# Kernel optimization log

Hardware: AMD Instinct MI355X
Metric: run time of the kernel (lower is better)

Reference implementation:

```python
import jax, jax.numpy as jnp
import numpy as np

B, N, F, W, K = 64, 1024, 5, 128, 2  # events, pulses/event, features, width, knn k
D2 = 2 * 3 * W  # 768 = 2*point_depth*width
NEG_SLOPE = 0.01
EPS = 1e-5


def setup_inputs() -> dict:
    key = jax.random.key(0)
    ks = jax.random.split(key, 16)
    def lin(k, fan_in, shape):
        return (jax.random.normal(k, shape, jnp.float32) / np.sqrt(fan_in)).astype(jnp.float32)
    return {
        "x": jax.random.normal(ks[0], (B, N, F), jnp.float32),
        # point1 MLP: Linear(2F->W), ReLU, Linear(W->W), ReLU
        "p1_w1": lin(ks[1], 2 * F, (2 * F, W)), "p1_b1": jnp.zeros((W,), jnp.float32),
        "p1_w2": lin(ks[2], W, (W, W)),       "p1_b2": jnp.zeros((W,), jnp.float32),
        # two pointfkt convs: Linear(2W->W), ReLU (stacked)
        "c_w": lin(ks[3], 2 * W, (2, 2 * W, W)), "c_b": jnp.zeros((2, W), jnp.float32),
        # BatchNorm1d(768)
        "bn_g": jnp.ones((D2,), jnp.float32), "bn_b": jnp.zeros((D2,), jnp.float32),
        # 5 Linear(768->768) (stacked)
        "lin_w": lin(ks[4], D2, (5, D2, D2)), "lin_b": jnp.zeros((5, D2), jnp.float32),
        # out: Linear(768->1)
        "out_w": lin(ks[5], D2, (D2, 1)), "out_b": jnp.zeros((1,), jnp.float32),
    }


def _knn_idx(x):
    # x: [B,N,D] -> indices of K nearest neighbors (incl. self), per event
    sq = jnp.sum(x * x, axis=-1)  # [B,N]
    dist = sq[:, :, None] + sq[:, None, :] - 2.0 * jnp.einsum('bnd,bmd->bnm', x, x)
    _, idx = jax.lax.top_k(-dist, K)  # [B,N,K]
    return idx


def _edge_feats(x, idx):
    # DGCNN edge features cat[x_i, x_j - x_i] -> [B,N,K,2D]
    xj = jax.vmap(lambda xb, ib: xb[ib])(x, idx)  # [B,N,K,D]
    xi = jnp.broadcast_to(x[:, :, None, :], xj.shape)
    return jnp.concatenate([xi, xj - xi], axis=-1)


def reference(x, p1_w1, p1_b1, p1_w2, p1_b2, c_w, c_b, bn_g, bn_b, lin_w, lin_b, out_w, out_b):
    # --- DynamicEdgeConv 1: MLP(2F->W->W), max-aggr over k neighbors ---
    e = _edge_feats(x, _knn_idx(x))                       # [B,N,K,2F]
    h = jax.nn.relu(jnp.einsum('bnkf,fw->bnkw', e, p1_w1) + p1_b1)
    h = jax.nn.relu(jnp.einsum('bnkw,wv->bnkv', h, p1_w2) + p1_b2)
    y = jnp.max(h, axis=2)                                # [B,N,W]
    pointlist = [y]
    # --- DynamicEdgeConv 2..point_depth: MLP(2W->W), max-aggr ---
    for f in range(2):
        e = _edge_feats(y, _knn_idx(y))                   # [B,N,K,2W]
        h = jax.nn.relu(jnp.einsum('bnkf,fw->bnkw', e, c_w[f]) + c_b[f])
        y = jnp.max(h, axis=2)
        pointlist.append(y)
    y = jnp.concatenate(pointlist, axis=-1)               # [B,N,3W]
    # global mean / max pool over nodes of each event -> [B,768]
    g = jnp.concatenate([jnp.mean(y, axis=1), jnp.max(y, axis=1)], axis=-1)
    # BatchNorm1d (training-mode batch statistics, biased variance)
    mu = jnp.mean(g, axis=0)
    var = jnp.mean((g - mu) ** 2, axis=0)
    h = (g - mu) * jax.lax.rsqrt(var + EPS) * bn_g + bn_b
    for i in range(5):
        h = jax.nn.leaky_relu(h @ lin_w[i] + lin_b[i], NEG_SLOPE)
    out = h @ out_w + out_b                               # [B,1]
    return out.reshape(-1)                                # [B]
```

## Files before the change

kernel.cpp:

```cpp
#include <hip/hip_runtime.h>
#include <cfloat>


typedef short short8 __attribute__((ext_vector_type(8)));
typedef float f32x4 __attribute__((ext_vector_type(4)));

__device__ __forceinline__ unsigned short f2bf(float f) {
  unsigned u = __float_as_uint(f);
  return (unsigned short)((u + 0x7fffu + ((u >> 16) & 1u)) >> 16);
}

__device__ __forceinline__ void top2_update(float& d1, int& j1, float& d2, int& j2,
                                            float dd, int j) {
  if (dd < d1 || (dd == d1 && j < j1)) { d2 = d1; j2 = j1; d1 = dd; j1 = j; }
  else if (dd < d2 || (dd == d2 && j < j2)) { d2 = dd; j2 = j; }
}

__device__ __forceinline__ void top2_merge_xor(float& d1, int& j1, float& d2, int& j2, int m) {
  float od1 = __shfl_xor(d1, m, 64); int oj1 = __shfl_xor(j1, m, 64);
  float od2 = __shfl_xor(d2, m, 64); int oj2 = __shfl_xor(j2, m, 64);
  bool aw = (d1 < od1) || (d1 == od1 && j1 < oj1);
  float h2d = aw ? d2 : od2;  int h2j = aw ? j2 : oj2;
  float lmd = aw ? od1 : d1;  int lmj = aw ? oj1 : j1;
  float nd1 = aw ? d1 : od1;  int nj1 = aw ? j1 : oj1;
  bool bw = (h2d < lmd) || (h2d == lmd && h2j < lmj);
  d1 = nd1; j1 = nj1;
  d2 = bw ? h2d : lmd; j2 = bw ? h2j : lmj;
}

__device__ __forceinline__ void top3_update(float& d1, int& j1, float& d2, int& j2,
                                            float& d3, int& j3, float dd, int j) {
  bool c1 = dd < d1, c2 = dd < d2, c3 = dd < d3;
  float n3 = c2 ? d2 : (c3 ? dd : d3); int m3 = c2 ? j2 : (c3 ? j : j3);
  float n2 = c1 ? d1 : (c2 ? dd : d2); int m2 = c1 ? j1 : (c2 ? j : j2);
  d1 = c1 ? dd : d1; j1 = c1 ? j : j1;
  d2 = n2; j2 = m2; d3 = n3; j3 = m3;
}

__global__ __launch_bounds__(256) void pn_split5(const float* __restrict__ x,
                                                 unsigned short* __restrict__ xh,
                                                 unsigned short* __restrict__ xl,
                                                 float* __restrict__ sq5) {
  int r = blockIdx.x * 256 + threadIdx.x;
  const float* xr = x + (size_t)r * 5;
  float v0 = xr[0], v1 = xr[1], v2 = xr[2], v3 = xr[3], v4 = xr[4];
  unsigned short h0 = f2bf(v0), h1 = f2bf(v1), h2 = f2bf(v2), h3 = f2bf(v3), h4 = f2bf(v4);
  unsigned short l0 = f2bf(v0 - __uint_as_float((unsigned)h0 << 16));
  unsigned short l1 = f2bf(v1 - __uint_as_float((unsigned)h1 << 16));
  unsigned short l2 = f2bf(v2 - __uint_as_float((unsigned)h2 << 16));
  unsigned short l3 = f2bf(v3 - __uint_as_float((unsigned)h3 << 16));
  unsigned short l4 = f2bf(v4 - __uint_as_float((unsigned)h4 << 16));
  uint4 Z = make_uint4(0u, 0u, 0u, 0u);
  uint4 H = make_uint4((unsigned)h0 | ((unsigned)h1 << 16),
                       (unsigned)h2 | ((unsigned)h3 << 16),
                       (unsigned)h4, 0u);
  uint4 L = make_uint4((unsigned)l0 | ((unsigned)l1 << 16),
                       (unsigned)l2 | ((unsigned)l3 << 16),
                       (unsigned)l4, 0u);
  uint4* dh = (uint4*)(xh + (size_t)r * 32);
  uint4* dl = (uint4*)(xl + (size_t)r * 32);
  dh[0] = H; dh[1] = Z; dh[2] = Z; dh[3] = Z;
  dl[0] = L; dl[1] = Z; dl[2] = Z; dl[3] = Z;
  sq5[r] = v0*v0 + v1*v1 + v2*v2 + v3*v3 + v4*v4;
}

__global__ __launch_bounds__(256) void pn_knn5_mfma(const unsigned short* __restrict__ Xh,
                                                    const unsigned short* __restrict__ Xl,
                                                    const float* __restrict__ sq5,
                                                    int4* __restrict__ cand) {
  __shared__ __align__(16) unsigned short Ah[128*40];
  __shared__ __align__(16) unsigned short Al[128*40];
  __shared__ __align__(16) unsigned short Bh[128*40];
  __shared__ __align__(16) unsigned short Bl[128*40];
  __shared__ float sqs[1024];
  int t = threadIdx.x;
  int b = blockIdx.x >> 3, it = blockIdx.x & 7, i0 = it * 128;
  int lane = t & 63, wave = t >> 6, quad = lane >> 4, l16 = lane & 15;
  #pragma unroll
  for (int s = 0; s < 4; ++s) sqs[t + 256*s] = sq5[b*1024 + t + 256*s];

  int sr = t >> 1, part = t & 1;
  {
    const uint4* sh = (const uint4*)&Xh[(size_t)(b*1024 + i0 + sr)*32 + part*16];
    const uint4* sl = (const uint4*)&Xl[(size_t)(b*1024 + i0 + sr)*32 + part*16];
    uint4* dh = (uint4*)&Ah[sr*40 + part*16];
    uint4* dl = (uint4*)&Al[sr*40 + part*16];
    dh[0] = sh[0]; dh[1] = sh[1];
    dl[0] = sl[0]; dl[1] = sl[1];
  }
  __syncthreads();
  short8 ah0 = *(const short8*)&Ah[(wave*32 + l16)*40 + quad*8];
  short8 ah1 = *(const short8*)&Ah[(wave*32 + 16 + l16)*40 + quad*8];
  short8 al0 = *(const short8*)&Al[(wave*32 + l16)*40 + quad*8];
  short8 al1 = *(const short8*)&Al[(wave*32 + 16 + l16)*40 + quad*8];

  float D1[8], D2[8], D3[8]; int J1[8], J2[8], J3[8];
  #pragma unroll
  for (int r = 0; r < 8; ++r) {
    D1[r] = FLT_MAX; D2[r] = FLT_MAX; D3[r] = FLT_MAX;
    J1[r] = 0x7fffffff; J2[r] = 0x7fffffff; J3[r] = 0x7fffffff;
  }

  #pragma unroll 1
  for (int jc = 0; jc < 8; ++jc) {
    __syncthreads();
    {
      const uint4* sh = (const uint4*)&Xh[(size_t)(b*1024 + jc*128 + sr)*32 + part*16];
      const uint4* sl = (const uint4*)&Xl[(size_t)(b*1024 + jc*128 + sr)*32 + part*16];
      uint4* dh = (uint4*)&Bh[sr*40 + part*16];
      uint4* dl = (uint4*)&Bl[sr*40 + part*16];
      dh[0] = sh[0]; dh[1] = sh[1];
      dl[0] = sl[0]; dl[1] = sl[1];
    }
    __syncthreads();
    f32x4 acc[2][8];
    #pragma unroll
    for (int s = 0; s < 2; ++s)
      #pragma unroll
      for (int js = 0; js < 8; ++js)
        acc[s][js] = (f32x4){0.f, 0.f, 0.f, 0.f};
    #pragma unroll
    for (int js = 0; js < 8; ++js) {
      short8 bh = *(const short8*)&Bh[(js*16 + l16)*40 + quad*8];
      short8 bl = *(const short8*)&Bl[(js*16 + l16)*40 + quad*8];
      acc[0][js] = __builtin_amdgcn_mfma_f32_16x16x32_bf16(ah0, bh, acc[0][js], 0, 0, 0);
      acc[0][js] = __builtin_amdgcn_mfma_f32_16x16x32_bf16(ah0, bl, acc[0][js], 0, 0, 0);
      acc[0][js] = __builtin_amdgcn_mfma_f32_16x16x32_bf16(al0, bh, acc[0][js], 0, 0, 0);
      acc[0][js] = __builtin_amdgcn_mfma_f32_16x16x32_bf16(al0, bl, acc[0][js], 0, 0, 0);
      acc[1][js] = __builtin_amdgcn_mfma_f32_16x16x32_bf16(ah1, bh, acc[1][js], 0, 0, 0);
      acc[1][js] = __builtin_amdgcn_mfma_f32_16x16x32_bf16(ah1, bl, acc[1][js], 0, 0, 0);
      acc[1][js] = __builtin_amdgcn_mfma_f32_16x16x32_bf16(al1, bh, acc[1][js], 0, 0, 0);
      acc[1][js] = __builtin_amdgcn_mfma_f32_16x16x32_bf16(al1, bl, acc[1][js], 0, 0, 0);
    }
    #pragma unroll
    for (int js = 0; js < 8; ++js) {
      int jg = jc*128 + js*16 + l16;
      float sj = sqs[jg];
      #pragma unroll
      for (int s = 0; s < 2; ++s)
        #pragma unroll
        for (int r = 0; r < 4; ++r) {
          float dd = fmaf(-2.f, acc[s][js][r], sj);
          int id8 = s*4 + r;
          top3_update(D1[id8], J1[id8], D2[id8], J2[id8], D3[id8], J3[id8], dd, jg);
        }
    }
  }

  #pragma unroll
  for (int id8 = 0; id8 < 8; ++id8) {
    #pragma unroll
    for (int m = 1; m < 16; m <<= 1) {
      float o1 = __shfl_xor(D1[id8], m, 64); int p1 = __shfl_xor(J1[id8], m, 64);
      float o2 = __shfl_xor(D2[id8], m, 64); int p2 = __shfl_xor(J2[id8], m, 64);
      float o3 = __shfl_xor(D3[id8], m, 64); int p3 = __shfl_xor(J3[id8], m, 64);
      top3_update(D1[id8], J1[id8], D2[id8], J2[id8], D3[id8], J3[id8], o1, p1);
      top3_update(D1[id8], J1[id8], D2[id8], J2[id8], D3[id8], J3[id8], o2, p2);
      top3_update(D1[id8], J1[id8], D2[id8], J2[id8], D3[id8], J3[id8], o3, p3);
    }
    if (l16 == 0) {
      int s = id8 >> 2, r = id8 & 3;
      int row = b*1024 + i0 + wave*32 + s*16 + quad*4 + r;
      cand[row] = make_int4(J1[id8], J2[id8], J3[id8], 0x7fffffff);
    }
  }
}

__global__ __launch_bounds__(256) void pn_knn5_rescore(const float* __restrict__ x,
                                                       const int4* __restrict__ cand,
                                                       int* __restrict__ idx) {
  int r = blockIdx.x * 256 + threadIdx.x;
  int base = (r >> 10) << 10;
  int4 cd = cand[r];
  const float* xi = x + (size_t)r * 5;
  float a0 = xi[0], a1 = xi[1], a2 = xi[2], a3 = xi[3], a4 = xi[4];
  float d1 = FLT_MAX, d2 = FLT_MAX; int j1 = 0x7fffffff, j2 = 0x7fffffff;
  int cs0 = cd.x, cs1 = cd.y, cs2 = cd.z;
  #pragma unroll
  for (int c = 0; c < 3; ++c) {
    int cj = (c == 0) ? cs0 : (c == 1) ? cs1 : cs2;
    const float* xj = x + (size_t)(base + cj) * 5;
    float f0 = xj[0] - a0, f1 = xj[1] - a1, f2 = xj[2] - a2,
          f3 = xj[3] - a3, f4 = xj[4] - a4;
    float dd = f0*f0 + f1*f1 + f2*f2 + f3*f3 + f4*f4;
    top2_update(d1, j1, d2, j2, dd, cj);
  }
  idx[r*2+0] = j1; idx[r*2+1] = j2;
}

__global__ __launch_bounds__(256) void pn_conv1_l1(const float* __restrict__ x,
                                                   const int* __restrict__ idx,
                                                   const float* __restrict__ w1,
                                                   const float* __restrict__ b1,
                                                   float* __restrict__ h1) {
  __shared__ float Ws[1280];
  __shared__ float Bs[128];
  __shared__ float xs[32][10];
  __shared__ int   js[32];
  int t = threadIdx.x;
  int r0 = blockIdx.x * 32;
  for (int s = t; s < 1280; s += 256) Ws[s] = w1[s];
  if (t < 128) Bs[t] = b1[t];
  if (t < 32) {
    int r = r0 + t; int i = r >> 1, k = r & 1;
    js[t] = idx[i*2 + k];
  }
  __syncthreads();
  for (int s = t; s < 320; s += 256) {
    int row = s / 10, f = s % 10;
    int r = r0 + row; int i = r >> 1;
    if (f < 5) xs[row][f] = x[(size_t)i * 5 + f];
    else {
      int jrow = ((i >> 10) << 10) + js[row];
      xs[row][f] = x[(size_t)jrow * 5 + (f - 5)];
    }
  }
  __syncthreads();
  int c = t & 127, rr = t >> 7;
  #pragma unroll
  for (int s = 0; s < 16; ++s) {
    int row = s * 2 + rr;
    float acc = Bs[c];
    #pragma unroll
    for (int f = 0; f < 5; ++f) {
      float a = xs[row][f];
      float d = xs[row][5+f] - a;
      acc = fmaf(a, Ws[f*128 + c], acc);
      acc = fmaf(d, Ws[(5+f)*128 + c], acc);
    }
    h1[(size_t)(r0 + row) * 128 + c] = fmaxf(acc, 0.0f);
  }
}

template<bool RELU, bool PAIRMAX>
__device__ __forceinline__ void gemm128_core(int bid, const float* __restrict__ A,
                                             const float* __restrict__ W,
                                             const float* __restrict__ bias,
                                             float* __restrict__ out) {
  __shared__ __align__(16) float As[4096];
  __shared__ __align__(16) float Wsb[32][132];
  int t = threadIdx.x;
  int rg = t >> 4;
  int cg = t & 15;
  float acc[8][8];
  #pragma unroll
  for (int a = 0; a < 8; ++a)
    #pragma unroll
    for (int b = 0; b < 8; ++b) acc[a][b] = 0.f;
  size_t r0 = (size_t)bid * 128;
  int ra = t >> 1, hf = t & 1;
  int wb = t >> 3, cp = t & 7;
  for (int w0 = 0; w0 < 128; w0 += 32) {
    const float* asrc = A + (r0 + ra) * 128 + w0 + hf * 16;
    #pragma unroll
    for (int q = 0; q < 4; ++q) {
      float4 v = ((const float4*)asrc)[q];
      int base = ((hf << 4) + (q << 2)) * 128 +
                 ((((ra >> 3) ^ ((hf << 2) + q)) << 3) | (ra & 7));
      As[base] = v.x; As[base+128] = v.y; As[base+256] = v.z; As[base+384] = v.w;
    }
    const float* wsrc = W + (size_t)(w0 + wb) * 128 + cp * 16;
    #pragma unroll
    for (int q = 0; q < 4; ++q)
      *(float4*)&Wsb[wb][cp*16 + q*4] = ((const float4*)wsrc)[q];
    __syncthreads();
    #pragma unroll
    for (int k4 = 0; k4 < 8; ++k4) {
      const float* pa = &As[(k4 << 9) + ((rg ^ k4) << 3)];
      #pragma unroll
      for (int kk = 0; kk < 4; ++kk) {
        int w = (k4 << 2) + kk;
        float4 a0 = *(const float4*)(pa + (kk << 7));
        float4 a1 = *(const float4*)(pa + (kk << 7) + 4);
        float4 wv0 = *(const float4*)&Wsb[w][cg*4];
        float4 wv1 = *(const float4*)&Wsb[w][64 + cg*4];
        float av[8] = {a0.x,a0.y,a0.z,a0.w,a1.x,a1.y,a1.z,a1.w};
        float wv[8] = {wv0.x,wv0.y,wv0.z,wv0.w,wv1.x,wv1.y,wv1.z,wv1.w};
        #pragma unroll
        for (int ri = 0; ri < 8; ++ri)
          #pragma unroll
          for (int ci = 0; ci < 8; ++ci)
            acc[ri][ci] = fmaf(av[ri], wv[ci], acc[ri][ci]);
      }
    }
    __syncthreads();
  }
  float blo[4], bhi[4];
  #pragma unroll
  for (int ci = 0; ci < 4; ++ci) {
    blo[ci] = bias ? bias[cg*4 + ci] : 0.f;
    bhi[ci] = bias ? bias[64 + cg*4 + ci] : 0.f;
  }
  if (PAIRMAX) {
    #pragma unroll
    for (int ri = 0; ri < 8; ri += 2) {
      size_t orow = (r0 + rg*8 + ri) >> 1;
      float lo[4], hi[4];
      #pragma unroll
      for (int ci = 0; ci < 4; ++ci) {
        float v0 = acc[ri][ci]   + blo[ci];
        float v1 = acc[ri+1][ci] + blo[ci];
        lo[ci] = fmaxf(fmaxf(v0, v1), 0.f);
        float w0v = acc[ri][ci+4]   + bhi[ci];
        float w1v = acc[ri+1][ci+4] + bhi[ci];
        hi[ci] = fmaxf(fmaxf(w0v, w1v), 0.f);
      }
      *(float4*)&out[orow*128 + cg*4]      = *(float4*)lo;
      *(float4*)&out[orow*128 + 64 + cg*4] = *(float4*)hi;
    }
  } else {
    #pragma unroll
    for (int ri = 0; ri < 8; ++ri) {
      size_t row = r0 + rg*8 + ri;
      float lo[4], hi[4];
      #pragma unroll
      for (int ci = 0; ci < 4; ++ci) {
        float v0 = acc[ri][ci]   + blo[ci];
        float v1 = acc[ri][ci+4] + bhi[ci];
        lo[ci] = RELU ? fmaxf(v0, 0.f) : v0;
        hi[ci] = RELU ? fmaxf(v1, 0.f) : v1;
      }
      *(float4*)&out[row*128 + cg*4]      = *(float4*)lo;
      *(float4*)&out[row*128 + 64 + cg*4] = *(float4*)hi;
    }
  }
}

__global__ __launch_bounds__(256) void pn_gemm128_bias(const float* __restrict__ A,
                                                       const float* __restrict__ W,
                                                       const float* __restrict__ bias,
                                                       float* __restrict__ out) {
  gemm128_core<true, true>(blockIdx.x, A, W, bias, out);
}

__global__ __launch_bounds__(256) void pn_gemm128_uv(const float* __restrict__ A,
                                                     const float* __restrict__ Wb,
                                                     float* __restrict__ U,
                                                     float* __restrict__ V) {
  int which = blockIdx.x >> 9;
  gemm128_core<false, false>(blockIdx.x & 511, A, Wb + (which << 14), nullptr,
                             which ? V : U);
}

__global__ __launch_bounds__(256) void pn_sqnorm(const float* __restrict__ y,
                                                 float* __restrict__ sq) {
  int r = blockIdx.x * 256 + threadIdx.x;
  const float4* p = (const float4*)(y + (size_t)r * 128);
  float s = 0.f;
  #pragma unroll
  for (int q = 0; q < 32; ++q) {
    float4 v = p[q];
    s += v.x*v.x + v.y*v.y + v.z*v.z + v.w*v.w;
  }
  sq[r] = s;
}

__global__ __launch_bounds__(256) void pn_split(const float* __restrict__ y,
                                                unsigned short* __restrict__ yh,
                                                unsigned short* __restrict__ yl) {
  int gid = blockIdx.x * 256 + threadIdx.x;
  float4 v = ((const float4*)y)[gid];
  ushort4 h, l;
  h.x = f2bf(v.x); l.x = f2bf(v.x - __uint_as_float((unsigned)h.x << 16));
  h.y = f2bf(v.y); l.y = f2bf(v.y - __uint_as_float((unsigned)h.y << 16));
  h.z = f2bf(v.z); l.z = f2bf(v.z - __uint_as_float((unsigned)h.z << 16));
  h.w = f2bf(v.w); l.w = f2bf(v.w - __uint_as_float((unsigned)h.w << 16));
  ((ushort4*)yh)[gid] = h;
  ((ushort4*)yl)[gid] = l;
}

__global__ __launch_bounds__(256) void pn_knn_mfma(const unsigned short* __restrict__ Yh,
                                                   const unsigned short* __restrict__ Yl,
                                                   const float* __restrict__ sqn,
                                                   int4* __restrict__ cand) {
  __shared__ __align__(16) unsigned short Ah[128*72];
  __shared__ __align__(16) unsigned short Al[128*72];
  __shared__ __align__(16) unsigned short Bh[128*72];
  __shared__ __align__(16) unsigned short Bl[128*72];
  __shared__ float sqs[1024];
  int t = threadIdx.x;
  int b  = blockIdx.x >> 3;
  int it = blockIdx.x & 7;
  int i0 = it * 128;
  int lane = t & 63, wave = t >> 6;
  int quad = lane >> 4, l16 = lane & 15;
  #pragma unroll
  for (int s = 0; s < 4; ++s) sqs[t + 256*s] = sqn[b*1024 + t + 256*s];

  float D1[8], D2[8], D3[8]; int J1[8], J2[8], J3[8];
  #pragma unroll
  for (int r = 0; r < 8; ++r) {
    D1[r] = FLT_MAX; D2[r] = FLT_MAX; D3[r] = FLT_MAX;
    J1[r] = 0x7fffffff; J2[r] = 0x7fffffff; J3[r] = 0x7fffffff;
  }

  int sr = t >> 1, shf = t & 1;

  #pragma unroll 1
  for (int jc = 0; jc < 8; ++jc) {
    f32x4 acc[2][8];
    #pragma unroll
    for (int s = 0; s < 2; ++s)
      #pragma unroll
      for (int js = 0; js < 8; ++js)
        acc[s][js] = (f32x4){0.f, 0.f, 0.f, 0.f};

    #pragma unroll 1
    for (int kc = 0; kc < 2; ++kc) {
      __syncthreads();
      {
        size_t ga = (size_t)(b*1024 + i0 + sr) * 128 + kc*64 + shf*32;
        size_t gb = (size_t)(b*1024 + jc*128 + sr) * 128 + kc*64 + shf*32;
        const uint4* sAh = (const uint4*)&Yh[ga];
        const uint4* sAl = (const uint4*)&Yl[ga];
        const uint4* sBh = (const uint4*)&Yh[gb];
        const uint4* sBl = (const uint4*)&Yl[gb];
        uint4* dAh = (uint4*)&Ah[sr*72 + shf*32];
        uint4* dAl = (uint4*)&Al[sr*72 + shf*32];
        uint4* dBh = (uint4*)&Bh[sr*72 + shf*32];
        uint4* dBl = (uint4*)&Bl[sr*72 + shf*32];
        #pragma unroll
        for (int q = 0; q < 4; ++q) {
          dAh[q] = sAh[q]; dAl[q] = sAl[q];
          dBh[q] = sBh[q]; dBl[q] = sBl[q];
        }
      }
      __syncthreads();
      #pragma unroll
      for (int ks = 0; ks < 2; ++ks) {
        int ko = ks*32 + quad*8;
        short8 ah0 = *(const short8*)&Ah[(wave*32 + l16)*72 + ko];
        short8 ah1 = *(const short8*)&Ah[(wave*32 + 16 + l16)*72 + ko];
        short8 al0 = *(const short8*)&Al[(wave*32 + l16)*72 + ko];
        short8 al1 = *(const short8*)&Al[(wave*32 + 16 + l16)*72 + ko];
        #pragma unroll
        for (int js = 0; js < 8; ++js) {
          short8 bh = *(const short8*)&Bh[(js*16 + l16)*72 + ko];
          short8 bl = *(const short8*)&Bl[(js*16 + l16)*72 + ko];
          acc[0][js] = __builtin_amdgcn_mfma_f32_16x16x32_bf16(ah0, bh, acc[0][js], 0, 0, 0);
          acc[0][js] = __builtin_amdgcn_mfma_f32_16x16x32_bf16(ah0, bl, acc[0][js], 0, 0, 0);
          acc[0][js] = __builtin_amdgcn_mfma_f32_16x16x32_bf16(al0, bh, acc[0][js], 0, 0, 0);
          acc[0][js] = __builtin_amdgcn_mfma_f32_16x16x32_bf16(al0, bl, acc[0][js], 0, 0, 0);
          acc[1][js] = __builtin_amdgcn_mfma_f32_16x16x32_bf16(ah1, bh, acc[1][js], 0, 0, 0);
          acc[1][js] = __builtin_amdgcn_mfma_f32_16x16x32_bf16(ah1, bl, acc[1][js], 0, 0, 0);
          acc[1][js] = __builtin_amdgcn_mfma_f32_16x16x32_bf16(al1, bh, acc[1][js], 0, 0, 0);
          acc[1][js] = __builtin_amdgcn_mfma_f32_16x16x32_bf16(al1, bl, acc[1][js], 0, 0, 0);
        }
      }
    }
    #pragma unroll
    for (int js = 0; js < 8; ++js) {
      int jg = jc*128 + js*16 + l16;
      float sj = sqs[jg];
      #pragma unroll
      for (int s = 0; s < 2; ++s)
        #pragma unroll
        for (int r = 0; r < 4; ++r) {
          float dd = fmaf(-2.f, acc[s][js][r], sj);
          int id8 = s*4 + r;
          top3_update(D1[id8], J1[id8], D2[id8], J2[id8], D3[id8], J3[id8], dd, jg);
        }
    }
  }

  #pragma unroll
  for (int id8 = 0; id8 < 8; ++id8) {
    #pragma unroll
    for (int m = 1; m < 16; m <<= 1) {
      float o1 = __shfl_xor(D1[id8], m, 64); int p1 = __shfl_xor(J1[id8], m, 64);
      float o2 = __shfl_xor(D2[id8], m, 64); int p2 = __shfl_xor(J2[id8], m, 64);
      float o3 = __shfl_xor(D3[id8], m, 64); int p3 = __shfl_xor(J3[id8], m, 64);
      top3_update(D1[id8], J1[id8], D2[id8], J2[id8], D3[id8], J3[id8], o1, p1);
      top3_update(D1[id8], J1[id8], D2[id8], J2[id8], D3[id8], J3[id8], o2, p2);
      top3_update(D1[id8], J1[id8], D2[id8], J2[id8], D3[id8], J3[id8], o3, p3);
    }
    if (l16 == 0) {
      int s = id8 >> 2, r = id8 & 3;
      int row = b*1024 + i0 + wave*32 + s*16 + quad*4 + r;
      cand[row] = make_int4(J1[id8], J2[id8], J3[id8], 0x7fffffff);
    }
  }
}

__global__ __launch_bounds__(256) void pn_knn_rescore(const float* __restrict__ Y,
                                                      const float* __restrict__ sqn,
                                                      const int4* __restrict__ cand,
                                                      int* __restrict__ idx) {
  int gid = blockIdx.x * 256 + threadIdx.x;
  int row = gid >> 2, c = gid & 3;
  int base = (row >> 10) << 10;
  int4 cd = cand[row];
  int cj = (c == 0) ? cd.x : (c == 1) ? cd.y : cd.z;
  const float4* yi = (const float4*)&Y[(size_t)row * 128];
  const float4* yj = (const float4*)&Y[(size_t)(base + cj) * 128];
  float acc = 0.f;
  #pragma unroll 8
  for (int q = 0; q < 32; ++q) {
    float4 a = yi[q], bq = yj[q];
    acc = fmaf(a.x, bq.x, acc);
    acc = fmaf(a.y, bq.y, acc);
    acc = fmaf(a.z, bq.z, acc);
    acc = fmaf(a.w, bq.w, acc);
  }
  float dd = sqn[row] + sqn[base + cj] - 2.0f * acc;
  int jv = cj;
  if (c == 3) { dd = FLT_MAX; jv = 0x7fffffff; }
  float d1 = dd, d2 = FLT_MAX; int j1 = jv, j2 = 0x7fffffff;
  top2_merge_xor(d1, j1, d2, j2, 1);
  top2_merge_xor(d1, j1, d2, j2, 2);
  if (c == 0) {
    idx[row*2+0] = j1;
    idx[row*2+1] = j2;
  }
}

__global__ __launch_bounds__(256) void pn_edge_max(const float* __restrict__ U,
                                                   const float* __restrict__ V,
                                                   const int* __restrict__ idx,
                                                   const float* __restrict__ bias,
                                                   float* __restrict__ y) {
  int gid = blockIdx.x * 256 + threadIdx.x;
  int i = gid >> 5, c4 = (gid & 31) << 2;
  int base = (i >> 10) << 10;
  int j0 = idx[i*2+0], j1 = idx[i*2+1];
  float4 u  = *(const float4*)&U[(size_t)i*128 + c4];
  float4 vi = *(const float4*)&V[(size_t)i*128 + c4];
  float4 v0 = *(const float4*)&V[(size_t)(base + j0)*128 + c4];
  float4 v1 = *(const float4*)&V[(size_t)(base + j1)*128 + c4];
  float4 bb = *(const float4*)&bias[c4];
  float4 o;
  o.x = fmaxf(fmaxf(u.x + v0.x - vi.x + bb.x, u.x + v1.x - vi.x + bb.x), 0.f);
  o.y = fmaxf(fmaxf(u.y + v0.y - vi.y + bb.y, u.y + v1.y - vi.y + bb.y), 0.f);
  o.z = fmaxf(fmaxf(u.z + v0.z - vi.z + bb.z, u.z + v1.z - vi.z + bb.z), 0.f);
  o.w = fmaxf(fmaxf(u.w + v0.w - vi.w + bb.w, u.w + v1.w - vi.w + bb.w), 0.f);
  *(float4*)&y[(size_t)i*128 + c4] = o;
}

__global__ __launch_bounds__(384) void pn_pool1(const float* __restrict__ y1,
                                                const float* __restrict__ y2,
                                                const float* __restrict__ y3,
                                                float* __restrict__ pp) {
  int b = blockIdx.x >> 2, ch = blockIdx.x & 3, c = threadIdx.x;
  const float* src = (c < 128) ? (y1 + (size_t)b * 131072 + c)
                   : (c < 256) ? (y2 + (size_t)b * 131072 + (c - 128))
                               : (y3 + (size_t)b * 131072 + (c - 256));
  src += (size_t)ch * 256 * 128;
  float s = 0.f, mx = -FLT_MAX;
  for (int n = 0; n < 256; ++n) {
    float v = src[(size_t)n * 128];
    s += v; mx = fmaxf(mx, v);
  }
  pp[(size_t)(b*4 + ch) * 768 + c] = s;
  pp[(size_t)(b*4 + ch) * 768 + 384 + c] = mx;
}

__global__ __launch_bounds__(384) void pn_pool2(const float* __restrict__ pp,
                                                float* __restrict__ g) {
  int b = blockIdx.x, c = threadIdx.x;
  float s = 0.f, mx = -FLT_MAX;
  #pragma unroll
  for (int ch = 0; ch < 4; ++ch) {
    s += pp[(size_t)(b*4 + ch) * 768 + c];
    mx = fmaxf(mx, pp[(size_t)(b*4 + ch) * 768 + 384 + c]);
  }
  g[b*768 + c] = s * (1.0f / 1024.0f);
  g[b*768 + 384 + c] = mx;
}

__global__ __launch_bounds__(256) void pn_bn(const float* __restrict__ g,
                                             const float* __restrict__ gamma,
                                             const float* __restrict__ beta,
                                             float* __restrict__ out) {
  int c = blockIdx.x * 256 + threadIdx.x;
  float mu = 0.f;
  for (int b = 0; b < 64; ++b) mu += g[b*768 + c];
  mu *= (1.0f / 64.0f);
  float var = 0.f;
  for (int b = 0; b < 64; ++b) { float d = g[b*768 + c] - mu; var += d * d; }
  var *= (1.0f / 64.0f);
  float sc = (1.0f / sqrtf(var + 1e-5f)) * gamma[c];
  float sh = beta[c];
  for (int b = 0; b < 64; ++b) out[b*768 + c] = (g[b*768 + c] - mu) * sc + sh;
}

__global__ __launch_bounds__(256) void pn_dense(const float* __restrict__ h,
                                                const float* __restrict__ W,
                                                const float* __restrict__ bias,
                                                float* __restrict__ out) {
  int b = blockIdx.x / 3;
  int c = (blockIdx.x % 3) * 256 + threadIdx.x;
  const float* hb = h + (size_t)b * 768;
  float a0 = bias[c], a1 = 0.f, a2 = 0.f, a3 = 0.f;
  for (int w = 0; w < 768; w += 4) {
    a0 = fmaf(hb[w+0], W[(size_t)(w+0)*768 + c], a0);
    a1 = fmaf(hb[w+1], W[(size_t)(w+1)*768 + c], a1);
    a2 = fmaf(hb[w+2], W[(size_t)(w+2)*768 + c], a2);
    a3 = fmaf(hb[w+3], W[(size_t)(w+3)*768 + c], a3);
  }
  float acc = (a0 + a1) + (a2 + a3);
  acc = acc > 0.f ? acc : 0.01f * acc;
  out[b*768 + c] = acc;
}

__global__ __launch_bounds__(256) void pn_out(const float* __restrict__ h,
                                              const float* __restrict__ ow,
                                              const float* __restrict__ ob,
                                              float* __restrict__ out) {
  int wid = blockIdx.x * 4 + (threadIdx.x >> 6);
  int lane = threadIdx.x & 63;
  const float* hb = h + (size_t)wid * 768;
  float s = 0.f;
  #pragma unroll
  for (int q = 0; q < 12; ++q) {
    int w = q * 64 + lane;
    s = fmaf(hb[w], ow[w], s);
  }
  #pragma unroll
  for (int m = 1; m < 64; m <<= 1) s += __shfl_xor(s, m, 64);
  if (lane == 0) out[wid] = s + ob[0];
}

extern "C" void kernel_launch(void* const* d_in, const int* in_sizes, int n_in,
                              void* d_out, int out_size, void* d_ws, size_t ws_size,
                              hipStream_t stream) {
  (void)in_sizes; (void)n_in; (void)out_size; (void)ws_size;
  const float* x     = (const float*)d_in[0];
  const float* p1w1  = (const float*)d_in[1];
  const float* p1b1  = (const float*)d_in[2];
  const float* p1w2  = (const float*)d_in[3];
  const float* p1b2  = (const float*)d_in[4];
  const float* cw    = (const float*)d_in[5];
  const float* cb    = (const float*)d_in[6];
  const float* bng   = (const float*)d_in[7];
  const float* bnb   = (const float*)d_in[8];
  const float* linw  = (const float*)d_in[9];
  const float* linb  = (const float*)d_in[10];
  const float* outw  = (const float*)d_in[11];
  const float* outb  = (const float*)d_in[12];
  float* outp = (float*)d_out;

  float* ws = (float*)d_ws;
  const size_t YSZ = (size_t)65536 * 128;
  float* y1 = ws;
  float* y2 = y1 + YSZ;
  float* y3 = y2 + YSZ;
  float* U  = y3 + YSZ;
  float* V  = U + YSZ;
  float* h1 = U;
  unsigned short* yh = (unsigned short*)U;
  unsigned short* yl = (unsigned short*)U + YSZ;
  unsigned short* xh5 = (unsigned short*)U;
  unsigned short* xl5 = xh5 + (size_t)65536 * 32;
  int4* cand = (int4*)V;
  float* sq = V + YSZ;
  int*   idxb = (int*)(sq + 65536);
  float* g  = (float*)(idxb + 131072);
  float* ha = g + 49152;
  float* hb = ha + 49152;
  float* pp = hb + 49152;

  pn_split5<<<256, 256, 0, stream>>>(x, xh5, xl5, sq);
  pn_knn5_mfma<<<512, 256, 0, stream>>>(xh5, xl5, sq, cand);
  pn_knn5_rescore<<<256, 256, 0, stream>>>(x, cand, idxb);
  pn_conv1_l1<<<4096, 256, 0, stream>>>(x, idxb, p1w1, p1b1, h1);
  pn_gemm128_bias<<<1024, 256, 0, stream>>>(h1, p1w2, p1b2, y1);
  pn_sqnorm<<<256, 256, 0, stream>>>(y1, sq);
  pn_split<<<8192, 256, 0, stream>>>(y1, yh, yl);
  pn_knn_mfma<<<512, 256, 0, stream>>>(yh, yl, sq, cand);
  pn_knn_rescore<<<1024, 256, 0, stream>>>(y1, sq, cand, idxb);
  pn_gemm128_uv<<<1024, 256, 0, stream>>>(y1, cw, U, V);
  pn_edge_max<<<8192, 256, 0, stream>>>(U, V, idxb, cb, y2);
  pn_sqnorm<<<256, 256, 0, stream>>>(y2, sq);
  pn_split<<<8192, 256, 0, stream>>>(y2, yh, yl);
  pn_knn_mfma<<<512, 256, 0, stream>>>(yh, yl, sq, cand);
  pn_knn_rescore<<<1024, 256, 0, stream>>>(y2, sq, cand, idxb);
  pn_gemm128_uv<<<1024, 256, 0, stream>>>(y2, cw + 32768, U, V);
  pn_edge_max<<<8192, 256, 0, stream>>>(U, V, idxb, cb + 128, y3);
  pn_pool1<<<256, 384, 0, stream>>>(y1, y2, y3, pp);
  pn_pool2<<<64, 384, 0, stream>>>(pp, g);
  pn_bn<<<3, 256, 0, stream>>>(g, bng, bnb, ha);
  pn_dense<<<192, 256, 0, stream>>>(ha, linw + 0*589824, linb + 0*768, hb);
  pn_dense<<<192, 256, 0, stream>>>(hb, linw + 1*589824, linb + 1*768, ha);
  pn_dense<<<192, 256, 0, stream>>>(ha, linw + 2*589824, linb + 2*768, hb);
  pn_dense<<<192, 256, 0, stream>>>(hb, linw + 3*589824, linb + 3*768, ha);
  pn_dense<<<192, 256, 0, stream>>>(ha, linw + 4*589824, linb + 4*768, hb);
  pn_out<<<16, 256, 0, stream>>>(hb, outw, outb, outp);
}
```

Before: 938.7 us.

## Shrink kNN MFMA row tile to 64 and keep A fragments in registers

The 128-dim kNN MFMA kernel now processes 64 query rows per block instead of 128, doubling the grid to 1024 blocks. Each wave loads its 16-row A fragments (hi/lo bf16) straight from global memory into registers once, so the A tiles are no longer staged through shared memory. This frees LDS and accumulator registers, which should raise occupancy and remove A staging traffic. The cost is that each B tile is reloaded from global memory by twice as many blocks, and each B tile in LDS is reused across fewer rows.

```diff
diff --git a/kernel.cpp b/kernel.cpp
--- a/kernel.cpp
+++ b/kernel.cpp
@@ -373,23 +373,31 @@
                                                    const unsigned short* __restrict__ Yl,
                                                    const float* __restrict__ sqn,
                                                    int4* __restrict__ cand) {
-  __shared__ __align__(16) unsigned short Ah[128*72];
-  __shared__ __align__(16) unsigned short Al[128*72];
   __shared__ __align__(16) unsigned short Bh[128*72];
   __shared__ __align__(16) unsigned short Bl[128*72];
   __shared__ float sqs[1024];
   int t = threadIdx.x;
-  int b  = blockIdx.x >> 3;
-  int it = blockIdx.x & 7;
-  int i0 = it * 128;
+  int b  = blockIdx.x >> 4;
+  int it = blockIdx.x & 15;
+  int i0 = it * 64;
   int lane = t & 63, wave = t >> 6;
   int quad = lane >> 4, l16 = lane & 15;
   #pragma unroll
   for (int s = 0; s < 4; ++s) sqs[t + 256*s] = sqn[b*1024 + t + 256*s];
 
-  float D1[8], D2[8], D3[8]; int J1[8], J2[8], J3[8];
-  #pragma unroll
-  for (int r = 0; r < 8; ++r) {
+  short8 ah[4], al[4];
+  {
+    size_t arow = (size_t)(b*1024 + i0 + wave*16 + l16) * 128;
+    #pragma unroll
+    for (int kg = 0; kg < 4; ++kg) {
+      ah[kg] = *(const short8*)&Yh[arow + kg*32 + quad*8];
+      al[kg] = *(const short8*)&Yl[arow + kg*32 + quad*8];
+    }
+  }
+
+  float D1[4], D2[4], D3[4]; int J1[4], J2[4], J3[4];
+  #pragma unroll
+  for (int r = 0; r < 4; ++r) {
     D1[r] = FLT_MAX; D2[r] = FLT_MAX; D3[r] = FLT_MAX;
     J1[r] = 0x7fffffff; J2[r] = 0x7fffffff; J3[r] = 0x7fffffff;
   }
@@ -398,53 +406,35 @@
 
   #pragma unroll 1
   for (int jc = 0; jc < 8; ++jc) {
-    f32x4 acc[2][8];
-    #pragma unroll
-    for (int s = 0; s < 2; ++s)
-      #pragma unroll
-      for (int js = 0; js < 8; ++js)
-        acc[s][js] = (f32x4){0.f, 0.f, 0.f, 0.f};
+    f32x4 acc[8];
+    #pragma unroll
+    for (int js = 0; js < 8; ++js) acc[js] = (f32x4){0.f, 0.f, 0.f, 0.f};
 
     #pragma unroll 1
     for (int kc = 0; kc < 2; ++kc) {
       __syncthreads();
       {
-        size_t ga = (size_t)(b*1024 + i0 + sr) * 128 + kc*64 + shf*32;
         size_t gb = (size_t)(b*1024 + jc*128 + sr) * 128 + kc*64 + shf*32;
-        const uint4* sAh = (const uint4*)&Yh[ga];
-        const uint4* sAl = (const uint4*)&Yl[ga];
         const uint4* sBh = (const uint4*)&Yh[gb];
         const uint4* sBl = (const uint4*)&Yl[gb];
-        uint4* dAh = (uint4*)&Ah[sr*72 + shf*32];
-        uint4* dAl = (uint4*)&Al[sr*72 + shf*32];
         uint4* dBh = (uint4*)&Bh[sr*72 + shf*32];
         uint4* dBl = (uint4*)&Bl[sr*72 + shf*32];
         #pragma unroll
-        for (int q = 0; q < 4; ++q) {
-          dAh[q] = sAh[q]; dAl[q] = sAl[q];
-          dBh[q] = sBh[q]; dBl[q] = sBl[q];
-        }
+        for (int q = 0; q < 4; ++q) { dBh[q] = sBh[q]; dBl[q] = sBl[q]; }
       }
       __syncthreads();
       #pragma unroll
       for (int ks = 0; ks < 2; ++ks) {
+        int kg = kc*2 + ks;
         int ko = ks*32 + quad*8;
-        short8 ah0 = *(const short8*)&Ah[(wave*32 + l16)*72 + ko];
-        short8 ah1 = *(const short8*)&Ah[(wave*32 + 16 + l16)*72 + ko];
-        short8 al0 = *(const short8*)&Al[(wave*32 + l16)*72 + ko];
-        short8 al1 = *(const short8*)&Al[(wave*32 + 16 + l16)*72 + ko];
         #pragma unroll
         for (int js = 0; js < 8; ++js) {
           short8 bh = *(const short8*)&Bh[(js*16 + l16)*72 + ko];
           short8 bl = *(const short8*)&Bl[(js*16 + l16)*72 + ko];
-          acc[0][js] = __builtin_amdgcn_mfma_f32_16x16x32_bf16(ah0, bh, acc[0][js], 0, 0, 0);
-          acc[0][js] = __builtin_amdgcn_mfma_f32_16x16x32_bf16(ah0, bl, acc[0][js], 0, 0, 0);
-          acc[0][js] = __builtin_amdgcn_mfma_f32_16x16x32_bf16(al0, bh, acc[0][js], 0, 0, 0);
-          acc[0][js] = __builtin_amdgcn_mfma_f32_16x16x32_bf16(al0, bl, acc[0][js], 0, 0, 0);
-          acc[1][js] = __builtin_amdgcn_mfma_f32_16x16x32_bf16(ah1, bh, acc[1][js], 0, 0, 0);
-          acc[1][js] = __builtin_amdgcn_mfma_f32_16x16x32_bf16(ah1, bl, acc[1][js], 0, 0, 0);
-          acc[1][js] = __builtin_amdgcn_mfma_f32_16x16x32_bf16(al1, bh, acc[1][js], 0, 0, 0);
-          acc[1][js] = __builtin_amdgcn_mfma_f32_16x16x32_bf16(al1, bl, acc[1][js], 0, 0, 0);
+          acc[js] = __builtin_amdgcn_mfma_f32_16x16x32_bf16(ah[kg], bh, acc[js], 0, 0, 0);
+          acc[js] = __builtin_amdgcn_mfma_f32_16x16x32_bf16(ah[kg], bl, acc[js], 0, 0, 0);
+          acc[js] = __builtin_amdgcn_mfma_f32_16x16x32_bf16(al[kg], bh, acc[js], 0, 0, 0);
+          acc[js] = __builtin_amdgcn_mfma_f32_16x16x32_bf16(al[kg], bl, acc[js], 0, 0, 0);
         }
       }
     }
@@ -453,31 +443,27 @@
       int jg = jc*128 + js*16 + l16;
       float sj = sqs[jg];
       #pragma unroll
-      for (int s = 0; s < 2; ++s)
-        #pragma unroll
-        for (int r = 0; r < 4; ++r) {
-          float dd = fmaf(-2.f, acc[s][js][r], sj);
-          int id8 = s*4 + r;
-          top3_update(D1[id8], J1[id8], D2[id8], J2[id8], D3[id8], J3[id8], dd, jg);
-        }
-    }
-  }
-
-  #pragma unroll
-  for (int id8 = 0; id8 < 8; ++id8) {
+      for (int r = 0; r < 4; ++r) {
+        float dd = fmaf(-2.f, acc[js][r], sj);
+        top3_update(D1[r], J1[r], D2[r], J2[r], D3[r], J3[r], dd, jg);
+      }
+    }
+  }
+
+  #pragma unroll
+  for (int r = 0; r < 4; ++r) {
     #pragma unroll
     for (int m = 1; m < 16; m <<= 1) {
-      float o1 = __shfl_xor(D1[id8], m, 64); int p1 = __shfl_xor(J1[id8], m, 64);
-      float o2 = __shfl_xor(D2[id8], m, 64); int p2 = __shfl_xor(J2[id8], m, 64);
-      float o3 = __shfl_xor(D3[id8], m, 64); int p3 = __shfl_xor(J3[id8], m, 64);
-      top3_update(D1[id8], J1[id8], D2[id8], J2[id8], D3[id8], J3[id8], o1, p1);
-      top3_update(D1[id8], J1[id8], D2[id8], J2[id8], D3[id8], J3[id8], o2, p2);
-      top3_update(D1[id8], J1[id8], D2[id8], J2[id8], D3[id8], J3[id8], o3, p3);
+      float o1 = __shfl_xor(D1[r], m, 64); int p1 = __shfl_xor(J1[r], m, 64);
+      float o2 = __shfl_xor(D2[r], m, 64); int p2 = __shfl_xor(J2[r], m, 64);
+      float o3 = __shfl_xor(D3[r], m, 64); int p3 = __shfl_xor(J3[r], m, 64);
+      top3_update(D1[r], J1[r], D2[r], J2[r], D3[r], J3[r], o1, p1);
+      top3_update(D1[r], J1[r], D2[r], J2[r], D3[r], J3[r], o2, p2);
+      top3_update(D1[r], J1[r], D2[r], J2[r], D3[r], J3[r], o3, p3);
     }
     if (l16 == 0) {
-      int s = id8 >> 2, r = id8 & 3;
-      int row = b*1024 + i0 + wave*32 + s*16 + quad*4 + r;
-      cand[row] = make_int4(J1[id8], J2[id8], J3[id8], 0x7fffffff);
+      int row = b*1024 + i0 + wave*16 + quad*4 + r;
+      cand[row] = make_int4(J1[r], J2[r], J3[r], 0x7fffffff);
     }
   }
 }
@@ -666,13 +652,13 @@
   pn_gemm128_bias<<<1024, 256, 0, stream>>>(h1, p1w2, p1b2, y1);
   pn_sqnorm<<<256, 256, 0, stream>>>(y1, sq);
   pn_split<<<8192, 256, 0, stream>>>(y1, yh, yl);
-  pn_knn_mfma<<<512, 256, 0, stream>>>(yh, yl, sq, cand);
+  pn_knn_mfma<<<1024, 256, 0, stream>>>(yh, yl, sq, cand);
   pn_knn_rescore<<<1024, 256, 0, stream>>>(y1, sq, cand, idxb);
   pn_gemm128_uv<<<1024, 256, 0, stream>>>(y1, cw, U, V);
   pn_edge_max<<<8192, 256, 0, stream>>>(U, V, idxb, cb, y2);
   pn_sqnorm<<<256, 256, 0, stream>>>(y2, sq);
   pn_split<<<8192, 256, 0, stream>>>(y2, yh, yl);
-  pn_knn_mfma<<<512, 256, 0, stream>>>(yh, yl, sq, cand);
+  pn_knn_mfma<<<1024, 256, 0, stream>>>(yh, yl, sq, cand);
   pn_knn_rescore<<<1024, 256, 0, stream>>>(y2, sq, cand, idxb);
   pn_gemm128_uv<<<1024, 256, 0, stream>>>(y2, cw + 32768, U, V);
   pn_edge_max<<<8192, 256, 0, stream>>>(U, V, idxb, cb + 128, y3);
```

After: 1.903 ms. 2.03x slower.
